# Optimization experiments

Hardware: AMD Instinct MI355X
Metric: run time of the kernel (lower is better)

The kernel has to match this reference:

```python
import math
import jax, jax.numpy as jnp
import numpy as np

B, T, C, H = 2, 2048, 1024, 16
D = C // H


def _slopes(n):
    def p2(m):
        start = 2 ** (-(2 ** -(math.log2(m) - 3)))
        return [start * start ** i for i in range(m)]
    if math.log2(n).is_integer():
        return p2(n)
    c = 2 ** math.floor(math.log2(n))
    return p2(c) + _slopes(2 * c)[0::2][: n - c]


def setup_inputs() -> dict:
    key = jax.random.key(0)
    ks = jax.random.split(key, 9)
    std = 0.02
    x = jax.random.normal(ks[0], (B, T, C), dtype=jnp.float32)
    Wq = std * jax.random.normal(ks[1], (C, C), dtype=jnp.float32)
    Wk = std * jax.random.normal(ks[2], (C, C), dtype=jnp.float32)
    Wv = std * jax.random.normal(ks[3], (C, C), dtype=jnp.float32)
    # fc_resid init: std 0.02/sqrt(num_layers)
    Wo = (std / math.sqrt(24.0)) * jax.random.normal(ks[4], (C, C), dtype=jnp.float32)
    bq = jnp.zeros((C,), jnp.float32)
    bk = jnp.zeros((C,), jnp.float32)
    bv = jnp.zeros((C,), jnp.float32)
    bo = jnp.zeros((C,), jnp.float32)
    return {"x": x, "Wq": Wq, "bq": bq, "Wk": Wk, "bk": bk,
            "Wv": Wv, "bv": bv, "Wo": Wo, "bo": bo}


def reference(x, Wq, bq, Wk, bk, Wv, bv, Wo, bo):
    # projections -> [B, T, H, D]
    q = (x @ Wq + bq).reshape(B, T, H, D)
    k = (x @ Wk + bk).reshape(B, T, H, D)
    v = (x @ Wv + bv).reshape(B, T, H, D)

    scale = 1.0 / math.sqrt(D)
    att = jnp.einsum("bqhd,bkhd->bhqk", q, k) * scale  # [B,H,T,T]

    slopes = jnp.asarray(_slopes(H), dtype=jnp.float32)  # [H]
    i = jnp.arange(T)
    rel = i[None, :] - i[None, :].T  # rel[i,j] = j - i
    causal = rel <= 0  # j <= i
    # alibi bias: -tril(i - j) = tril(j - i), scaled per head
    alibi = slopes[:, None, None] * jnp.where(causal, rel, 0).astype(jnp.float32)

    att = att + alibi[None]  # broadcast over batch
    att = jnp.where(causal[None, None], att, -jnp.inf)
    att = jax.nn.softmax(att, axis=-1)

    y = jnp.einsum("bhqk,bkhd->bqhd", att, v).reshape(B, T, C)
    return y @ Wo + bo  # dropout p=0 (eval) is identity
```

## Files before the change

kernel.cpp:

```cpp
#include <hip/hip_runtime.h>
#include <hip/hip_bf16.h>

typedef __bf16 bf16;
typedef __bf16 bf16x4 __attribute__((ext_vector_type(4)));
typedef __bf16 bf16x8 __attribute__((ext_vector_type(8)));
typedef float floatx4 __attribute__((ext_vector_type(4)));
typedef short short4_ __attribute__((ext_vector_type(4)));

#define B_ 2
#define T_ 2048
#define C_ 1024
#define H_ 16
#define D_ 64
#define M_ 4096
#define QK_LD 2048

__device__ __forceinline__ void load_lds16(const void* g, void* l) {
  __builtin_amdgcn_global_load_lds(
      (const __attribute__((address_space(1))) unsigned int*)g,
      (__attribute__((address_space(3))) unsigned int*)l, 16, 0, 0);
}

__device__ __forceinline__ floatx4 mfma16(bf16x4 a, bf16x4 b, floatx4 c) {
#if __has_builtin(__builtin_amdgcn_mfma_f32_16x16x16_bf16)
  return __builtin_amdgcn_mfma_f32_16x16x16_bf16(a, b, c, 0, 0, 0);
#else
  return __builtin_amdgcn_mfma_f32_16x16x16bf16_1k(
      __builtin_bit_cast(short4_, a), __builtin_bit_cast(short4_, b), c, 0, 0, 0);
#endif
}

__device__ __forceinline__ bf16x4 lo4(bf16x8 v) {
  return __builtin_shufflevector(v, v, 0, 1, 2, 3);
}
__device__ __forceinline__ bf16x4 hi4(bf16x8 v) {
  return __builtin_shufflevector(v, v, 4, 5, 6, 7);
}

struct PrepArgs { const float* w[4]; bf16* wt[4]; const float* x; bf16* xb; };

__global__ __launch_bounds__(256)
void prep(PrepArgs p) {
  const int bid = blockIdx.x;
  if (bid < 4096) {
    __shared__ float tile[32][33];
    const int z = bid >> 10, xy = bid & 1023;
    const int bx = xy & 31, by = xy >> 5;
    const float* in = p.w[z];
    bf16* out = p.wt[z];
    int tx = threadIdx.x & 31, ty = threadIdx.x >> 5;
    int n0 = bx * 32, k0 = by * 32;
#pragma unroll
    for (int j = 0; j < 32; j += 8)
      tile[ty + j][tx] = in[(size_t)(k0 + ty + j) * C_ + n0 + tx];
    __syncthreads();
#pragma unroll
    for (int j = 0; j < 32; j += 8)
      out[(size_t)(n0 + ty + j) * C_ + k0 + tx] = (bf16)tile[tx][ty + j];
  } else {
    int i = ((bid - 4096) * 256 + threadIdx.x) * 8;
    float4 a = *(const float4*)(p.x + i);
    float4 b = *(const float4*)(p.x + i + 4);
    bf16x8 o;
    o[0] = (bf16)a.x; o[1] = (bf16)a.y; o[2] = (bf16)a.z; o[3] = (bf16)a.w;
    o[4] = (bf16)b.x; o[5] = (bf16)b.y; o[6] = (bf16)b.z; o[7] = (bf16)b.w;
    *(bf16x8*)(p.xb + i) = o;
  }
}

struct GQ {
  const bf16* A; const bf16* Bt;
  const float* bias[3];
  bf16* Cout; bf16* vt; int N; int K;
};

__global__ __launch_bounds__(256, 2)
void gemm128(GQ g) {
  __shared__ __align__(16) bf16 As[128 * 64];
  __shared__ __align__(16) bf16 Bs[128 * 64];
  const int tid = threadIdx.x;
  const int wave = tid >> 6, lane = tid & 63;
  const int quad = lane >> 4, l16 = lane & 15;
  const int m0 = blockIdx.y * 128, n0 = blockIdx.x * 128;
  const int wm = (wave >> 1) * 64, wn = (wave & 1) * 64;

  floatx4 acc[4][4] = {};

  int rA[4], cA[4];
#pragma unroll
  for (int t = 0; t < 4; ++t) {
    int pch = (wave * 4 + t) * 64 + lane;
    rA[t] = pch >> 3;
    cA[t] = (pch & 7) ^ (rA[t] & 7);
  }

  for (int k0 = 0; k0 < g.K; k0 += 64) {
    __syncthreads();
#pragma unroll
    for (int t = 0; t < 4; ++t) {
      load_lds16(g.A + (size_t)(m0 + rA[t]) * g.K + k0 + cA[t] * 8,
                 As + (wave * 4 + t) * 512);
      load_lds16(g.Bt + (size_t)(n0 + rA[t]) * g.K + k0 + cA[t] * 8,
                 Bs + (wave * 4 + t) * 512);
    }
    __builtin_amdgcn_s_waitcnt(0x0f70);
    __syncthreads();
#pragma unroll
    for (int s = 0; s < 2; ++s) {
      bf16x8 af[4], bfr[4];
#pragma unroll
      for (int i = 0; i < 4; ++i) {
        int mr = wm + i * 16 + l16;
        af[i] = *(const bf16x8*)(As + ((mr * 8) + ((s * 4 + quad) ^ (mr & 7))) * 8);
        int nr = wn + i * 16 + l16;
        bfr[i] = *(const bf16x8*)(Bs + ((nr * 8) + ((s * 4 + quad) ^ (nr & 7))) * 8);
      }
#pragma unroll
      for (int i = 0; i < 4; ++i)
#pragma unroll
        for (int j = 0; j < 4; ++j)
          acc[i][j] = __builtin_amdgcn_mfma_f32_16x16x32_bf16(af[i], bfr[j],
                                                              acc[i][j], 0, 0, 0);
    }
  }

  const bool vsplit = (n0 >= 2048);
#pragma unroll
  for (int j = 0; j < 4; ++j) {
    int col = n0 + wn + j * 16 + l16;
    const float* bp = g.bias[col >> 10];
    float bv = bp[col & 1023];
    if (vsplit) {
      int cv = col - 2048;
      bf16* dstb = g.vt + ((size_t)((m0 >> 11) * 16 + (cv >> 6)) * 64 + (cv & 63)) * (size_t)T_
                   + (m0 & 2047) + wm + quad * 8;
#pragma unroll
      for (int ii = 0; ii < 2; ++ii) {
        bf16x8 pk;
#pragma unroll
        for (int r = 0; r < 8; ++r)
          pk[r] = (bf16)(acc[ii * 2 + (r >> 2)][j][r & 3] + bv);
        *(bf16x8*)(dstb + ii * 32) = pk;
      }
    } else {
#pragma unroll
      for (int i = 0; i < 4; ++i) {
#pragma unroll
        for (int r = 0; r < 4; ++r) {
          int row = m0 + wm + i * 16 + quad * 4 + r;
          g.Cout[(size_t)row * g.N + col] = (bf16)(acc[i][j][r] + bv);
        }
      }
    }
  }
}

__global__ __launch_bounds__(256, 2)
void gemm_out(const bf16* __restrict__ A, const bf16* __restrict__ Bt,
              const float* __restrict__ bias, float* __restrict__ C) {
  __shared__ __align__(16) bf16 As[64 * 64];
  __shared__ __align__(16) bf16 Bs[128 * 64];
  const int tid = threadIdx.x;
  const int wave = tid >> 6, lane = tid & 63;
  const int quad = lane >> 4, l16 = lane & 15;
  const int m0 = blockIdx.y * 64, n0 = blockIdx.x * 128;
  const int wm = (wave >> 1) * 32, wn = (wave & 1) * 64;

  floatx4 acc[2][4] = {};

  int rA[2], cA[2], rB[4], cB[4];
#pragma unroll
  for (int t = 0; t < 2; ++t) {
    int p = t * 256 + tid;
    rA[t] = p >> 3; cA[t] = (p & 7) ^ (rA[t] & 7);
  }
#pragma unroll
  for (int t = 0; t < 4; ++t) {
    int p = t * 256 + tid;
    rB[t] = p >> 3; cB[t] = (p & 7) ^ (rB[t] & 7);
  }

  for (int k0 = 0; k0 < 1024; k0 += 64) {
    __syncthreads();
#pragma unroll
    for (int t = 0; t < 2; ++t)
      load_lds16(A + (size_t)(m0 + rA[t]) * 1024 + k0 + cA[t] * 8,
                 As + t * 2048 + wave * 512);
#pragma unroll
    for (int t = 0; t < 4; ++t)
      load_lds16(Bt + (size_t)(n0 + rB[t]) * 1024 + k0 + cB[t] * 8,
                 Bs + t * 2048 + wave * 512);
    __builtin_amdgcn_s_waitcnt(0x0f70);
    __syncthreads();
#pragma unroll
    for (int s = 0; s < 2; ++s) {
      bf16x8 af[2], bfr[4];
#pragma unroll
      for (int i = 0; i < 2; ++i) {
        int mr = wm + i * 16 + l16;
        af[i] = *(const bf16x8*)(As + ((mr * 8) + ((s * 4 + quad) ^ (mr & 7))) * 8);
      }
#pragma unroll
      for (int j = 0; j < 4; ++j) {
        int nr = wn + j * 16 + l16;
        bfr[j] = *(const bf16x8*)(Bs + ((nr * 8) + ((s * 4 + quad) ^ (nr & 7))) * 8);
      }
#pragma unroll
      for (int i = 0; i < 2; ++i)
#pragma unroll
        for (int j = 0; j < 4; ++j)
          acc[i][j] = __builtin_amdgcn_mfma_f32_16x16x32_bf16(af[i], bfr[j],
                                                              acc[i][j], 0, 0, 0);
    }
  }

#pragma unroll
  for (int j = 0; j < 4; ++j) {
    int col = n0 + wn + j * 16 + l16;
    float bv = bias[col];
#pragma unroll
    for (int i = 0; i < 2; ++i)
#pragma unroll
      for (int r = 0; r < 4; ++r) {
        int row = m0 + wm + i * 16 + quad * 4 + r;
        C[(size_t)row * 1024 + col] = acc[i][j][r] + bv;
      }
  }
}

__constant__ int yy_map[24] = {7, 8, 16, 9, 17, 6, 10, 18, 11, 19, 5, 12,
                               20, 13, 21, 4, 14, 22, 15, 23, 3, 2, 1, 0};

__global__ __launch_bounds__(512, 2)
void attn8(const bf16* __restrict__ qk, const bf16* __restrict__ vt,
           bf16* __restrict__ y, bf16* __restrict__ po, float* __restrict__ pl) {
  __shared__ __align__(16) bf16 smem[32768];
  const int tid = threadIdx.x, wave = tid >> 6, lane = tid & 63;
  const int quad = lane >> 4, l16 = lane & 15;
  const int qs = wave >> 1, kh = wave & 1;
  const int id = blockIdx.x;
  const int pos = id >> 3;
  const int bh = (id & 7) * 4 + (pos & 3);
  const int b = bh >> 4, h = bh & 15;
  const int yy = yy_map[pos >> 2];
  int qb, kbeg, kcnt, seg;
  if (yy < 8)       { qb = yy;      kbeg = 0;      kcnt = 2 * qb + 2; seg = -1; }
  else if (yy < 16) { qb = 23 - yy; kbeg = 0;      kcnt = qb + 1;     seg = 0;  }
  else              { qb = 31 - yy; kbeg = qb + 1; kcnt = qb + 1;     seg = 1;  }

  const float L2E = 1.4426950408889634f;
  const float slope2 = exp2f(-0.5f * (float)(h + 1)) * L2E;
  const float scl2 = 0.125f * L2E;
  const float M0 = 14.0f;

  const int rS = tid >> 3;
  const int cS = (tid & 7) ^ (rS & 7);
  const bf16* kbase = qk + (size_t)b * T_ * QK_LD + 1024 + h * 64;
  const bf16* vbase = vt + (size_t)bh * 64 * T_;

  const int q0 = qb * 128;
  const int w0 = q0 + qs * 32;

  bf16x8 qf[2][2];
#pragma unroll
  for (int qt = 0; qt < 2; ++qt)
#pragma unroll
    for (int s = 0; s < 2; ++s)
      qf[qt][s] = *(const bf16x8*)(qk +
          (size_t)(b * T_ + w0 + qt * 16 + l16) * QK_LD + h * 64 + s * 32 + quad * 8);

  const int qi0 = w0 + l16;
  float qoff[2];
  qoff[0] = slope2 * (float)qi0 + M0;
  qoff[1] = qoff[0] + slope2 * 16.0f;
  float kc[2][4];
#pragma unroll
  for (int kt = 0; kt < 2; ++kt)
#pragma unroll
    for (int r = 0; r < 4; ++r)
      kc[kt][r] = slope2 * (float)(kt * 16 + quad * 4 + r);

  floatx4 o[2][4];
#pragma unroll
  for (int qt = 0; qt < 2; ++qt)
#pragma unroll
    for (int n = 0; n < 4; ++n) o[qt][n] = (floatx4)0.f;
  float lsum[2] = {0.f, 0.f};

  auto tilebody = [&](const bf16* Klc, const bf16* Vlc, int tile) {
    const int kj0 = (kbeg + tile) * 64;
    bf16x8 kf[2][2];
#pragma unroll
    for (int ss = 0; ss < 2; ++ss)
#pragma unroll
      for (int kt = 0; kt < 2; ++kt) {
        const int krow = kh * 32 + kt * 16 + l16;
        kf[ss][kt] = *(const bf16x8*)(Klc + krow * 64 +
                                      (((ss * 4 + quad) ^ (krow & 7)) * 8));
      }
    bf16x8 vf8[4];
#pragma unroll
    for (int nt = 0; nt < 4; ++nt) {
      const int drow = nt * 16 + l16;
      vf8[nt] = *(const bf16x8*)(Vlc + drow * 64 +
                                 (((kh * 4 + quad) ^ (drow & 7)) * 8));
    }

    const int kbi = kj0 + kh * 32;
    const float kb = slope2 * (float)kbi;

    __builtin_amdgcn_s_setprio(1);
#pragma unroll
    for (int qt = 0; qt < 2; ++qt) {
      const int rb = w0 + qt * 16;
      floatx4 st[2] = {};
#pragma unroll
      for (int ss = 0; ss < 2; ++ss)
#pragma unroll
        for (int kt = 0; kt < 2; ++kt)
          st[kt] = __builtin_amdgcn_mfma_f32_16x16x32_bf16(kf[ss][kt], qf[qt][ss],
                                                           st[kt], 0, 0, 0);

      const float bb = kb - qoff[qt];
      const int qi = qi0 + qt * 16;
      bf16x4 pb[2];
      if (kbi + 31 > rb) {
#pragma unroll
        for (int kt = 0; kt < 2; ++kt) {
#pragma unroll
          for (int r = 0; r < 4; ++r) {
            float p = __builtin_amdgcn_exp2f(
                fmaf(st[kt][r], scl2, bb + kc[kt][r]));
            if (kbi + kt * 16 + quad * 4 + r > qi) p = 0.f;
            lsum[qt] += p;
            pb[kt][r] = (bf16)p;
          }
        }
      } else {
#pragma unroll
        for (int kt = 0; kt < 2; ++kt) {
#pragma unroll
          for (int r = 0; r < 4; ++r) {
            float p = __builtin_amdgcn_exp2f(
                fmaf(st[kt][r], scl2, bb + kc[kt][r]));
            lsum[qt] += p;
            pb[kt][r] = (bf16)p;
          }
        }
      }

#pragma unroll
      for (int nt = 0; nt < 4; ++nt) {
        o[qt][nt] = mfma16(lo4(vf8[nt]), pb[0], o[qt][nt]);
        o[qt][nt] = mfma16(hi4(vf8[nt]), pb[1], o[qt][nt]);
      }
    }
    __builtin_amdgcn_s_setprio(0);
  };

#pragma unroll
  for (int s2 = 0; s2 < 2; ++s2) {
    load_lds16(kbase + (size_t)((kbeg + s2) * 64 + rS) * QK_LD + cS * 8,
               smem + s2 * 4096 + wave * 512);
    load_lds16(vbase + (size_t)rS * T_ + (kbeg + s2) * 64 + cS * 8,
               smem + 16384 + s2 * 4096 + wave * 512);
  }
  __builtin_amdgcn_s_waitcnt(0x0f70);
  __syncthreads();

  const int npair = kcnt >> 1;
  const int nit = (kcnt + 1) >> 1;
  for (int it = 0; it < npair; ++it) {
    const int cur = it & 1;

    if (it + 1 < nit) {
      const int nt0 = kbeg + 2 * it + 2;
#pragma unroll
      for (int s2 = 0; s2 < 2; ++s2) {
        load_lds16(kbase + (size_t)((nt0 + s2) * 64 + rS) * QK_LD + cS * 8,
                   smem + (cur ^ 1) * 8192 + s2 * 4096 + wave * 512);
        load_lds16(vbase + (size_t)rS * T_ + (nt0 + s2) * 64 + cS * 8,
                   smem + 16384 + (cur ^ 1) * 8192 + s2 * 4096 + wave * 512);
      }
    }

    tilebody(smem + cur * 8192,        smem + 16384 + cur * 8192,        2 * it);
    tilebody(smem + cur * 8192 + 4096, smem + 16384 + cur * 8192 + 4096, 2 * it + 1);

    __builtin_amdgcn_s_waitcnt(0x0f70);
    __syncthreads();
  }
  if (kcnt & 1) {
    const int cur = npair & 1;
    tilebody(smem + cur * 8192, smem + 16384 + cur * 8192, kcnt - 1);
    __syncthreads();
  }

  float* Cb = (float*)smem;
  if (kh == 1) {
#pragma unroll
    for (int qt = 0; qt < 2; ++qt) {
#pragma unroll
      for (int n = 0; n < 4; ++n)
        *(floatx4*)(Cb + (((qs * 2 + qt) * 4 + n) * 64 + lane) * 4) = o[qt][n];
      Cb[8192 + (qs * 2 + qt) * 64 + lane] = lsum[qt];
    }
  }
  __syncthreads();
  if (kh == 1) return;
#pragma unroll
  for (int qt = 0; qt < 2; ++qt) {
#pragma unroll
    for (int n = 0; n < 4; ++n)
      o[qt][n] += *(const floatx4*)(Cb + (((qs * 2 + qt) * 4 + n) * 64 + lane) * 4);
    lsum[qt] += Cb[8192 + (qs * 2 + qt) * 64 + lane];
    lsum[qt] += __shfl_xor(lsum[qt], 16);
    lsum[qt] += __shfl_xor(lsum[qt], 32);
  }

  if (seg < 0) {
#pragma unroll
    for (int qt = 0; qt < 2; ++qt) {
      const float inv = 1.f / lsum[qt];
      bf16* yp = y + (size_t)(b * T_ + w0 + qt * 16 + l16) * C_ + h * 64 + quad * 4;
#pragma unroll
      for (int nt = 0; nt < 4; ++nt) {
        bf16x4 pk;
#pragma unroll
        for (int r = 0; r < 4; ++r) pk[r] = (bf16)(o[qt][nt][r] * inv);
        *(bf16x4*)(yp + nt * 16) = pk;
      }
    }
  } else {
    const int pid = (bh * 8 + (qb - 8)) * 2 + seg;
    bf16* pob = po + (size_t)pid * 8192;
#pragma unroll
    for (int qt = 0; qt < 2; ++qt) {
#pragma unroll
      for (int half = 0; half < 2; ++half) {
        bf16x8 pk;
#pragma unroll
        for (int jj = 0; jj < 8; ++jj)
          pk[jj] = (bf16)o[qt][half * 2 + (jj >> 2)][jj & 3];
        *(bf16x8*)(pob + (qt * 2 + half) * 2048 + (qs * 64 + lane) * 8) = pk;
      }
      if (quad == 0)
        pl[pid * 128 + qs * 32 + qt * 16 + l16] = lsum[qt];
    }
  }
}

__global__ __launch_bounds__(256)
void combine(const bf16* __restrict__ po, const float* __restrict__ pl,
             bf16* __restrict__ y) {
  const int x = blockIdx.x;
  const int bh = x >> 3, qb = (x & 7) + 8;
  const int b = bh >> 4, h = bh & 15;
  const int pid0 = (bh * 8 + (qb - 8)) * 2;
  const bf16* p0 = po + (size_t)pid0 * 8192;
  const bf16* p1 = p0 + 8192;
  const int t = threadIdx.x;
  const int qs = t >> 6, quad = (t >> 4) & 3, l16 = t & 15;

  float linv[2];
  int row[2];
#pragma unroll
  for (int qt = 0; qt < 2; ++qt) {
    row[qt] = qs * 32 + qt * 16 + l16;
    linv[qt] = 1.f / (pl[pid0 * 128 + row[qt]] + pl[(pid0 + 1) * 128 + row[qt]]);
  }

#pragma unroll
  for (int qt = 0; qt < 2; ++qt)
#pragma unroll
    for (int half = 0; half < 2; ++half) {
      bf16x8 a = *(const bf16x8*)(p0 + (qt * 2 + half) * 2048 + t * 8);
      bf16x8 c = *(const bf16x8*)(p1 + (qt * 2 + half) * 2048 + t * 8);
#pragma unroll
      for (int g = 0; g < 2; ++g) {
        bf16x4 outv;
#pragma unroll
        for (int r = 0; r < 4; ++r)
          outv[r] = (bf16)(((float)a[g * 4 + r] + (float)c[g * 4 + r]) * linv[qt]);
        const int col = (half * 2 + g) * 16 + quad * 4;
        *(bf16x4*)(y + (size_t)(b * T_ + qb * 128 + row[qt]) * C_ + h * 64 + col) = outv;
      }
    }
}

extern "C" void kernel_launch(void* const* d_in, const int* in_sizes, int n_in,
                              void* d_out, int out_size, void* d_ws, size_t ws_size,
                              hipStream_t stream) {
  const float* x  = (const float*)d_in[0];
  const float* Wq = (const float*)d_in[1];
  const float* bq = (const float*)d_in[2];
  const float* Wk = (const float*)d_in[3];
  const float* bk = (const float*)d_in[4];
  const float* Wv = (const float*)d_in[5];
  const float* bv = (const float*)d_in[6];
  const float* Wo = (const float*)d_in[7];
  const float* bo = (const float*)d_in[8];

  bf16* ws  = (bf16*)d_ws;
  bf16* WtQ = ws;
  bf16* WtK = WtQ + (size_t)C_ * C_;
  bf16* WtV = WtK + (size_t)C_ * C_;
  bf16* WtO = WtV + (size_t)C_ * C_;
  bf16* xb  = WtO + (size_t)C_ * C_;
  bf16* qkb = xb + (size_t)M_ * C_;
  bf16* vtb = qkb + (size_t)M_ * 2 * C_;
  bf16* yb  = vtb + (size_t)M_ * C_;
  bf16* pob = yb + (size_t)M_ * C_;
  float* plb = (float*)(pob + (size_t)512 * 8192);

  PrepArgs pp;
  pp.w[0] = Wq; pp.w[1] = Wk; pp.w[2] = Wv; pp.w[3] = Wo;
  pp.wt[0] = WtQ; pp.wt[1] = WtK; pp.wt[2] = WtV; pp.wt[3] = WtO;
  pp.x = x; pp.xb = xb;
  prep<<<dim3(4096 + M_ * C_ / (256 * 8)), 256, 0, stream>>>(pp);

  GQ gq;
  gq.A = xb; gq.Bt = WtQ;
  gq.bias[0] = bq; gq.bias[1] = bk; gq.bias[2] = bv;
  gq.Cout = qkb; gq.vt = vtb; gq.N = 2 * C_; gq.K = C_;
  gemm128<<<dim3(24, 32), 256, 0, stream>>>(gq);

  attn8<<<dim3(768), 512, 0, stream>>>(qkb, vtb, yb, pob, plb);
  combine<<<dim3(32 * 8), 256, 0, stream>>>(pob, plb, yb);

  gemm_out<<<dim3(8, 64), 256, 0, stream>>>(yb, WtO, bo, (float*)d_out);
}
```

Measured before the change: 175.1 us.

## Rebalance causal attention work into 512 equal-cost blocks with two-phase role pairing

Replaces the 768-block lookup-table schedule with 512 blocks. Each block either processes a short query block paired with the tail segment of a long query block, or the head segment of a long block, so every block covers about 17-18 key tiles. The goal is to even out per-block work and cut the tail imbalance of causal attention on the device. It also accumulates the row sums per register lane, which shortens the serial add dependency. In exchange, some blocks run two sequential phases with an extra sync and a second Q load, and the split point for long query blocks moves.

```diff
diff --git a/kernel.cpp b/kernel.cpp
--- a/kernel.cpp
+++ b/kernel.cpp
@@ -228,9 +228,6 @@
   }
 }
 
-__constant__ int yy_map[24] = {7, 8, 16, 9, 17, 6, 10, 18, 11, 19, 5, 12,
-                               20, 13, 21, 4, 14, 22, 15, 23, 3, 2, 1, 0};
-
 __global__ __launch_bounds__(512, 2)
 void attn8(const bf16* __restrict__ qk, const bf16* __restrict__ vt,
            bf16* __restrict__ y, bf16* __restrict__ po, float* __restrict__ pl) {
@@ -239,14 +236,11 @@
   const int quad = lane >> 4, l16 = lane & 15;
   const int qs = wave >> 1, kh = wave & 1;
   const int id = blockIdx.x;
-  const int pos = id >> 3;
-  const int bh = (id & 7) * 4 + (pos & 3);
+  const int bh = (id & 7) * 4 + ((id >> 3) & 3);
+  const int rem = id >> 5;
+  const int p = rem >> 1;
+  const bool roleB = rem & 1;
   const int b = bh >> 4, h = bh & 15;
-  const int yy = yy_map[pos >> 2];
-  int qb, kbeg, kcnt, seg;
-  if (yy < 8)       { qb = yy;      kbeg = 0;      kcnt = 2 * qb + 2; seg = -1; }
-  else if (yy < 16) { qb = 23 - yy; kbeg = 0;      kcnt = qb + 1;     seg = 0;  }
-  else              { qb = 31 - yy; kbeg = qb + 1; kcnt = qb + 1;     seg = 1;  }
 
   const float L2E = 1.4426950408889634f;
   const float slope2 = exp2f(-0.5f * (float)(h + 1)) * L2E;
@@ -258,21 +252,6 @@
   const bf16* kbase = qk + (size_t)b * T_ * QK_LD + 1024 + h * 64;
   const bf16* vbase = vt + (size_t)bh * 64 * T_;
 
-  const int q0 = qb * 128;
-  const int w0 = q0 + qs * 32;
-
-  bf16x8 qf[2][2];
-#pragma unroll
-  for (int qt = 0; qt < 2; ++qt)
-#pragma unroll
-    for (int s = 0; s < 2; ++s)
-      qf[qt][s] = *(const bf16x8*)(qk +
-          (size_t)(b * T_ + w0 + qt * 16 + l16) * QK_LD + h * 64 + s * 32 + quad * 8);
-
-  const int qi0 = w0 + l16;
-  float qoff[2];
-  qoff[0] = slope2 * (float)qi0 + M0;
-  qoff[1] = qoff[0] + slope2 * 16.0f;
   float kc[2][4];
 #pragma unroll
   for (int kt = 0; kt < 2; ++kt)
@@ -280,173 +259,202 @@
     for (int r = 0; r < 4; ++r)
       kc[kt][r] = slope2 * (float)(kt * 16 + quad * 4 + r);
 
-  floatx4 o[2][4];
-#pragma unroll
-  for (int qt = 0; qt < 2; ++qt)
-#pragma unroll
-    for (int n = 0; n < 4; ++n) o[qt][n] = (floatx4)0.f;
-  float lsum[2] = {0.f, 0.f};
-
-  auto tilebody = [&](const bf16* Klc, const bf16* Vlc, int tile) {
-    const int kj0 = (kbeg + tile) * 64;
-    bf16x8 kf[2][2];
-#pragma unroll
-    for (int ss = 0; ss < 2; ++ss)
-#pragma unroll
-      for (int kt = 0; kt < 2; ++kt) {
-        const int krow = kh * 32 + kt * 16 + l16;
-        kf[ss][kt] = *(const bf16x8*)(Klc + krow * 64 +
-                                      (((ss * 4 + quad) ^ (krow & 7)) * 8));
-      }
-    bf16x8 vf8[4];
-#pragma unroll
-    for (int nt = 0; nt < 4; ++nt) {
-      const int drow = nt * 16 + l16;
-      vf8[nt] = *(const bf16x8*)(Vlc + drow * 64 +
-                                 (((kh * 4 + quad) ^ (drow & 7)) * 8));
-    }
-
-    const int kbi = kj0 + kh * 32;
-    const float kb = slope2 * (float)kbi;
-
-    __builtin_amdgcn_s_setprio(1);
-#pragma unroll
-    for (int qt = 0; qt < 2; ++qt) {
-      const int rb = w0 + qt * 16;
-      floatx4 st[2] = {};
+  int qb_ = roleB ? (15 - p) : p;
+  int t0_ = 0;
+  int t1_ = roleB ? 17 : (2 * p + 2);
+  int sg_ = roleB ? 0 : -1;
+
+  for (int ph = 0;; ++ph) {
+    const int w0 = qb_ * 128 + qs * 32;
+    const int qi0 = w0 + l16;
+    float qoff[2];
+    qoff[0] = slope2 * (float)qi0 + M0;
+    qoff[1] = qoff[0] + slope2 * 16.0f;
+
+    bf16x8 qf[2][2];
+#pragma unroll
+    for (int qt = 0; qt < 2; ++qt)
+#pragma unroll
+      for (int s = 0; s < 2; ++s)
+        qf[qt][s] = *(const bf16x8*)(qk +
+            (size_t)(b * T_ + w0 + qt * 16 + l16) * QK_LD + h * 64 + s * 32 + quad * 8);
+
+    floatx4 o[2][4];
+#pragma unroll
+    for (int qt = 0; qt < 2; ++qt)
+#pragma unroll
+      for (int n = 0; n < 4; ++n) o[qt][n] = (floatx4)0.f;
+    floatx4 lsv[2];
+    lsv[0] = (floatx4)0.f; lsv[1] = (floatx4)0.f;
+
+    auto tilebody = [&](const bf16* Klc, const bf16* Vlc, int t) {
+      const int kj0 = t * 64;
+      bf16x8 kf[2][2];
 #pragma unroll
       for (int ss = 0; ss < 2; ++ss)
 #pragma unroll
-        for (int kt = 0; kt < 2; ++kt)
-          st[kt] = __builtin_amdgcn_mfma_f32_16x16x32_bf16(kf[ss][kt], qf[qt][ss],
-                                                           st[kt], 0, 0, 0);
-
-      const float bb = kb - qoff[qt];
-      const int qi = qi0 + qt * 16;
-      bf16x4 pb[2];
-      if (kbi + 31 > rb) {
-#pragma unroll
         for (int kt = 0; kt < 2; ++kt) {
-#pragma unroll
-          for (int r = 0; r < 4; ++r) {
-            float p = __builtin_amdgcn_exp2f(
-                fmaf(st[kt][r], scl2, bb + kc[kt][r]));
-            if (kbi + kt * 16 + quad * 4 + r > qi) p = 0.f;
-            lsum[qt] += p;
-            pb[kt][r] = (bf16)p;
+          const int krow = kh * 32 + kt * 16 + l16;
+          kf[ss][kt] = *(const bf16x8*)(Klc + krow * 64 +
+                                        (((ss * 4 + quad) ^ (krow & 7)) * 8));
+        }
+      bf16x8 vf8[4];
+#pragma unroll
+      for (int nt = 0; nt < 4; ++nt) {
+        const int drow = nt * 16 + l16;
+        vf8[nt] = *(const bf16x8*)(Vlc + drow * 64 +
+                                   (((kh * 4 + quad) ^ (drow & 7)) * 8));
+      }
+
+      const int kbi = kj0 + kh * 32;
+      const float kb = slope2 * (float)kbi;
+
+      __builtin_amdgcn_s_setprio(1);
+#pragma unroll
+      for (int qt = 0; qt < 2; ++qt) {
+        const int rb = w0 + qt * 16;
+        floatx4 st[2] = {};
+#pragma unroll
+        for (int ss = 0; ss < 2; ++ss)
+#pragma unroll
+          for (int kt = 0; kt < 2; ++kt)
+            st[kt] = __builtin_amdgcn_mfma_f32_16x16x32_bf16(kf[ss][kt], qf[qt][ss],
+                                                             st[kt], 0, 0, 0);
+
+        const float bb = kb - qoff[qt];
+        const int qi = qi0 + qt * 16;
+        bf16x4 pb[2];
+        if (kbi + 31 > rb) {
+#pragma unroll
+          for (int kt = 0; kt < 2; ++kt) {
+#pragma unroll
+            for (int r = 0; r < 4; ++r) {
+              float pv = __builtin_amdgcn_exp2f(
+                  fmaf(st[kt][r], scl2, bb + kc[kt][r]));
+              if (kbi + kt * 16 + quad * 4 + r > qi) pv = 0.f;
+              lsv[qt][r] += pv;
+              pb[kt][r] = (bf16)pv;
+            }
           }
+        } else {
+#pragma unroll
+          for (int kt = 0; kt < 2; ++kt) {
+#pragma unroll
+            for (int r = 0; r < 4; ++r) {
+              float pv = __builtin_amdgcn_exp2f(
+                  fmaf(st[kt][r], scl2, bb + kc[kt][r]));
+              lsv[qt][r] += pv;
+              pb[kt][r] = (bf16)pv;
+            }
+          }
+        }
+
+#pragma unroll
+        for (int nt = 0; nt < 4; ++nt) {
+          o[qt][nt] = mfma16(lo4(vf8[nt]), pb[0], o[qt][nt]);
+          o[qt][nt] = mfma16(hi4(vf8[nt]), pb[1], o[qt][nt]);
+        }
+      }
+      __builtin_amdgcn_s_setprio(0);
+    };
+
+#pragma unroll
+    for (int s2 = 0; s2 < 2; ++s2) {
+      load_lds16(kbase + (size_t)((t0_ + s2) * 64 + rS) * QK_LD + cS * 8,
+                 smem + s2 * 4096 + wave * 512);
+      load_lds16(vbase + (size_t)rS * T_ + (t0_ + s2) * 64 + cS * 8,
+                 smem + 16384 + s2 * 4096 + wave * 512);
+    }
+    __builtin_amdgcn_s_waitcnt(0x0f70);
+    __syncthreads();
+
+    const int len = t1_ - t0_;
+    const int npair = len >> 1;
+    const int nit = (len + 1) >> 1;
+    for (int it = 0; it < npair; ++it) {
+      const int cur = it & 1;
+      if (it + 1 < nit) {
+        const int nt0 = t0_ + 2 * it + 2;
+#pragma unroll
+        for (int s2 = 0; s2 < 2; ++s2) {
+          load_lds16(kbase + (size_t)((nt0 + s2) * 64 + rS) * QK_LD + cS * 8,
+                     smem + (cur ^ 1) * 8192 + s2 * 4096 + wave * 512);
+          load_lds16(vbase + (size_t)rS * T_ + (nt0 + s2) * 64 + cS * 8,
+                     smem + 16384 + (cur ^ 1) * 8192 + s2 * 4096 + wave * 512);
+        }
+      }
+      tilebody(smem + cur * 8192,        smem + 16384 + cur * 8192,        t0_ + 2 * it);
+      tilebody(smem + cur * 8192 + 4096, smem + 16384 + cur * 8192 + 4096, t0_ + 2 * it + 1);
+      __builtin_amdgcn_s_waitcnt(0x0f70);
+      __syncthreads();
+    }
+    if (len & 1) {
+      const int cur = npair & 1;
+      tilebody(smem + cur * 8192, smem + 16384 + cur * 8192, t1_ - 1);
+      __syncthreads();
+    }
+
+    float* Cb = (float*)smem;
+    float lsum[2];
+#pragma unroll
+    for (int qt = 0; qt < 2; ++qt)
+      lsum[qt] = (lsv[qt][0] + lsv[qt][1]) + (lsv[qt][2] + lsv[qt][3]);
+    if (kh == 1) {
+#pragma unroll
+      for (int qt = 0; qt < 2; ++qt) {
+#pragma unroll
+        for (int n = 0; n < 4; ++n)
+          *(floatx4*)(Cb + (((qs * 2 + qt) * 4 + n) * 64 + lane) * 4) = o[qt][n];
+        Cb[8192 + (qs * 2 + qt) * 64 + lane] = lsum[qt];
+      }
+    }
+    __syncthreads();
+    if (kh == 0) {
+#pragma unroll
+      for (int qt = 0; qt < 2; ++qt) {
+#pragma unroll
+        for (int n = 0; n < 4; ++n)
+          o[qt][n] += *(const floatx4*)(Cb + (((qs * 2 + qt) * 4 + n) * 64 + lane) * 4);
+        lsum[qt] += Cb[8192 + (qs * 2 + qt) * 64 + lane];
+        lsum[qt] += __shfl_xor(lsum[qt], 16);
+        lsum[qt] += __shfl_xor(lsum[qt], 32);
+      }
+
+      if (sg_ < 0) {
+#pragma unroll
+        for (int qt = 0; qt < 2; ++qt) {
+          const float inv = 1.f / lsum[qt];
+          bf16* yp = y + (size_t)(b * T_ + w0 + qt * 16 + l16) * C_ + h * 64 + quad * 4;
+#pragma unroll
+          for (int nt = 0; nt < 4; ++nt) {
+            bf16x4 pk;
+#pragma unroll
+            for (int r = 0; r < 4; ++r) pk[r] = (bf16)(o[qt][nt][r] * inv);
+            *(bf16x4*)(yp + nt * 16) = pk;
+          }
         }
       } else {
-#pragma unroll
-        for (int kt = 0; kt < 2; ++kt) {
-#pragma unroll
-          for (int r = 0; r < 4; ++r) {
-            float p = __builtin_amdgcn_exp2f(
-                fmaf(st[kt][r], scl2, bb + kc[kt][r]));
-            lsum[qt] += p;
-            pb[kt][r] = (bf16)p;
+        const int pid = (bh * 8 + (qb_ - 8)) * 2 + sg_;
+        bf16* pob = po + (size_t)pid * 8192;
+#pragma unroll
+        for (int qt = 0; qt < 2; ++qt) {
+#pragma unroll
+          for (int half = 0; half < 2; ++half) {
+            bf16x8 pk;
+#pragma unroll
+            for (int jj = 0; jj < 8; ++jj)
+              pk[jj] = (bf16)o[qt][half * 2 + (jj >> 2)][jj & 3];
+            *(bf16x8*)(pob + (qt * 2 + half) * 2048 + (qs * 64 + lane) * 8) = pk;
           }
-        }
-      }
-
-#pragma unroll
-      for (int nt = 0; nt < 4; ++nt) {
-        o[qt][nt] = mfma16(lo4(vf8[nt]), pb[0], o[qt][nt]);
-        o[qt][nt] = mfma16(hi4(vf8[nt]), pb[1], o[qt][nt]);
-      }
-    }
-    __builtin_amdgcn_s_setprio(0);
-  };
-
-#pragma unroll
-  for (int s2 = 0; s2 < 2; ++s2) {
-    load_lds16(kbase + (size_t)((kbeg + s2) * 64 + rS) * QK_LD + cS * 8,
-               smem + s2 * 4096 + wave * 512);
-    load_lds16(vbase + (size_t)rS * T_ + (kbeg + s2) * 64 + cS * 8,
-               smem + 16384 + s2 * 4096 + wave * 512);
-  }
-  __builtin_amdgcn_s_waitcnt(0x0f70);
-  __syncthreads();
-
-  const int npair = kcnt >> 1;
-  const int nit = (kcnt + 1) >> 1;
-  for (int it = 0; it < npair; ++it) {
-    const int cur = it & 1;
-
-    if (it + 1 < nit) {
-      const int nt0 = kbeg + 2 * it + 2;
-#pragma unroll
-      for (int s2 = 0; s2 < 2; ++s2) {
-        load_lds16(kbase + (size_t)((nt0 + s2) * 64 + rS) * QK_LD + cS * 8,
-                   smem + (cur ^ 1) * 8192 + s2 * 4096 + wave * 512);
-        load_lds16(vbase + (size_t)rS * T_ + (nt0 + s2) * 64 + cS * 8,
-                   smem + 16384 + (cur ^ 1) * 8192 + s2 * 4096 + wave * 512);
-      }
-    }
-
-    tilebody(smem + cur * 8192,        smem + 16384 + cur * 8192,        2 * it);
-    tilebody(smem + cur * 8192 + 4096, smem + 16384 + cur * 8192 + 4096, 2 * it + 1);
-
-    __builtin_amdgcn_s_waitcnt(0x0f70);
-    __syncthreads();
-  }
-  if (kcnt & 1) {
-    const int cur = npair & 1;
-    tilebody(smem + cur * 8192, smem + 16384 + cur * 8192, kcnt - 1);
-    __syncthreads();
-  }
-
-  float* Cb = (float*)smem;
-  if (kh == 1) {
-#pragma unroll
-    for (int qt = 0; qt < 2; ++qt) {
-#pragma unroll
-      for (int n = 0; n < 4; ++n)
-        *(floatx4*)(Cb + (((qs * 2 + qt) * 4 + n) * 64 + lane) * 4) = o[qt][n];
-      Cb[8192 + (qs * 2 + qt) * 64 + lane] = lsum[qt];
-    }
-  }
-  __syncthreads();
-  if (kh == 1) return;
-#pragma unroll
-  for (int qt = 0; qt < 2; ++qt) {
-#pragma unroll
-    for (int n = 0; n < 4; ++n)
-      o[qt][n] += *(const floatx4*)(Cb + (((qs * 2 + qt) * 4 + n) * 64 + lane) * 4);
-    lsum[qt] += Cb[8192 + (qs * 2 + qt) * 64 + lane];
-    lsum[qt] += __shfl_xor(lsum[qt], 16);
-    lsum[qt] += __shfl_xor(lsum[qt], 32);
-  }
-
-  if (seg < 0) {
-#pragma unroll
-    for (int qt = 0; qt < 2; ++qt) {
-      const float inv = 1.f / lsum[qt];
-      bf16* yp = y + (size_t)(b * T_ + w0 + qt * 16 + l16) * C_ + h * 64 + quad * 4;
-#pragma unroll
-      for (int nt = 0; nt < 4; ++nt) {
-        bf16x4 pk;
-#pragma unroll
-        for (int r = 0; r < 4; ++r) pk[r] = (bf16)(o[qt][nt][r] * inv);
-        *(bf16x4*)(yp + nt * 16) = pk;
-      }
-    }
-  } else {
-    const int pid = (bh * 8 + (qb - 8)) * 2 + seg;
-    bf16* pob = po + (size_t)pid * 8192;
-#pragma unroll
-    for (int qt = 0; qt < 2; ++qt) {
-#pragma unroll
-      for (int half = 0; half < 2; ++half) {
-        bf16x8 pk;
-#pragma unroll
-        for (int jj = 0; jj < 8; ++jj)
-          pk[jj] = (bf16)o[qt][half * 2 + (jj >> 2)][jj & 3];
-        *(bf16x8*)(pob + (qt * 2 + half) * 2048 + (qs * 64 + lane) * 8) = pk;
-      }
-      if (quad == 0)
-        pl[pid * 128 + qs * 32 + qt * 16 + l16] = lsum[qt];
-    }
+          if (quad == 0)
+            pl[pid * 128 + qs * 32 + qt * 16 + l16] = lsum[qt];
+        }
+      }
+    }
+    __syncthreads();
+
+    if (roleB || ph == 1) break;
+    qb_ = 15 - p; t0_ = 17; t1_ = 32 - 2 * p; sg_ = 1;
   }
 }
 
@@ -525,7 +533,7 @@
   gq.Cout = qkb; gq.vt = vtb; gq.N = 2 * C_; gq.K = C_;
   gemm128<<<dim3(24, 32), 256, 0, stream>>>(gq);
 
-  attn8<<<dim3(768), 512, 0, stream>>>(qkb, vtb, yb, pob, plb);
+  attn8<<<dim3(512), 512, 0, stream>>>(qkb, vtb, yb, pob, plb);
   combine<<<dim3(32 * 8), 256, 0, stream>>>(pob, plb, yb);
 
   gemm_out<<<dim3(8, 64), 256, 0, stream>>>(yb, WtO, bo, (float*)d_out);
```

New measurement: 178.8 us. 1.02x slower.
